# Kernel tuning notes

Measured on AMD Instinct MI355X. Metric: run time of the kernel, lower is better.

## Reference

```python
import jax, jax.numpy as jnp
import numpy as np

N = 100000      # nodes per batched graph
E = 3200000     # edges per batched graph
G = 1024        # number of graphs in the batch
F_IN = 128
H = 64


def gcn_conv(x, src, dst, W, b, n):
    # PyG GCNConv: lin -> symmetric-normalized propagate (with self-loops) -> +bias
    xw = x @ W                                   # [n, out]
    deg = jnp.zeros((n,), x.dtype).at[dst].add(1.0) + 1.0   # A+I degree
    dinv = jax.lax.rsqrt(deg)                    # deg >= 1, safe
    norm = (dinv[src] * dinv[dst])[:, None]      # [E,1]
    agg = jax.ops.segment_sum(norm * xw[src], dst, num_segments=n)
    # self-loop contribution: dinv[i]^2 * xw[i]
    return agg + (dinv * dinv)[:, None] * xw + b


def mean_pool(h, batch, num_graphs):
    sums = jax.ops.segment_sum(h, batch, num_segments=num_graphs)
    cnt = jax.ops.segment_sum(jnp.ones((h.shape[0],), h.dtype), batch, num_segments=num_graphs)
    return sums / jnp.maximum(cnt, 1.0)[:, None]


def branch(x, edge_index, batch, W1, b1, W2, b2):
    src, dst = edge_index[0], edge_index[1]
    h = jax.nn.relu(gcn_conv(x, src, dst, W1, b1, x.shape[0]))
    h = jax.nn.relu(gcn_conv(h, src, dst, W2, b2, x.shape[0]))
    return mean_pool(h, batch, G)


def setup_inputs() -> dict:
    key = jax.random.key(0)
    ks = jax.random.split(key, 14)
    x1 = jax.random.normal(ks[0], (N, F_IN), jnp.float32)
    x2 = jax.random.normal(ks[1], (N, F_IN), jnp.float32)
    edge_index1 = jax.random.randint(ks[2], (2, E), 0, N, jnp.int32)
    edge_index2 = jax.random.randint(ks[3], (2, E), 0, N, jnp.int32)
    batch1 = jnp.sort(jax.random.randint(ks[4], (N,), 0, G, jnp.int32))
    batch2 = jnp.sort(jax.random.randint(ks[5], (N,), 0, G, jnp.int32))
    s = 1.0 / np.sqrt(F_IN)
    W1 = jax.random.uniform(ks[6], (F_IN, H), jnp.float32, -s, s)
    b1 = jnp.zeros((H,), jnp.float32)
    s2 = 1.0 / np.sqrt(H)
    W2 = jax.random.uniform(ks[7], (H, H), jnp.float32, -s2, s2)
    b2 = jnp.zeros((H,), jnp.float32)
    s3 = 1.0 / np.sqrt(3 * H)
    fc1_W = jax.random.uniform(ks[8], (3 * H, H), jnp.float32, -s3, s3)
    fc1_b = jax.random.uniform(ks[9], (H,), jnp.float32, -s3, s3)
    fc2_W = jax.random.uniform(ks[10], (H, 1), jnp.float32, -s2, s2)
    fc2_b = jax.random.uniform(ks[11], (1,), jnp.float32, -s2, s2)
    return {"x1": x1, "edge_index1": edge_index1, "batch1": batch1,
            "x2": x2, "edge_index2": edge_index2, "batch2": batch2,
            "W1": W1, "b1": b1, "W2": W2, "b2": b2,
            "fc1_W": fc1_W, "fc1_b": fc1_b, "fc2_W": fc2_W, "fc2_b": fc2_b}


def reference(x1, edge_index1, batch1, x2, edge_index2, batch2,
              W1, b1, W2, b2, fc1_W, fc1_b, fc2_W, fc2_b):
    emb1 = branch(x1, edge_index1, batch1, W1, b1, W2, b2)   # [G, 64]
    emb2 = branch(x2, edge_index2, batch2, W1, b1, W2, b2)   # [G, 64]
    combined = jnp.concatenate([emb1, emb2, jnp.abs(emb1 - emb2)], axis=1)  # [G, 192]
    out = jax.nn.relu(combined @ fc1_W + fc1_b)
    out = jax.nn.sigmoid(out @ fc2_W + fc2_b)
    return out.squeeze(-1)  # [G]
```

## Files before the change

### kernel.cpp

```cpp
#include <hip/hip_runtime.h>
#include <hip/hip_fp16.h>
#include <cstdint>


#define NBSH 8
#define CAPB 10240
#define SPLIT_T 512
#define SPLIT_EPT 28
#define SPLIT_CHUNK (SPLIT_T * SPLIT_EPT)

__device__ __forceinline__ float fatomic(float* p, float v) {
    return unsafeAtomicAdd(p, v);
}
__device__ __forceinline__ float bf2f(unsigned short u) {
    union { unsigned int i; float f; } c; c.i = ((unsigned int)u) << 16; return c.f;
}
__device__ __forceinline__ unsigned short f2bf(float f) {
    union { float f; unsigned int i; } c; c.f = f;
    const unsigned int b = c.i;
    return (unsigned short)((b + 0x7FFF + ((b >> 16) & 1)) >> 16);
}

#if defined(__has_builtin)
#if __has_builtin(__builtin_amdgcn_cvt_f32_fp8) && __has_builtin(__builtin_amdgcn_cvt_pk_fp8_f32)
#define HW_FP8 1
#endif
#endif

__device__ __forceinline__ float fp8dec(unsigned int b) {
#ifdef HW_FP8
    return __builtin_amdgcn_cvt_f32_fp8((int)b, 0);
#else
    const unsigned int mag = (b & 0x7Fu) << 20;
    const float f = __uint_as_float(mag) * __uint_as_float(0x7B800000u);
    const unsigned int r = __float_as_uint(f) | ((b & 0x80u) << 24);
    return __uint_as_float(r);
#endif
}

__device__ __forceinline__ unsigned char fp8enc(float x) {
#ifdef HW_FP8
    const int v = __builtin_amdgcn_cvt_pk_fp8_f32(x, x, 0, false);
    return (unsigned char)(v & 0xFF);
#else
    const unsigned short h = __half_as_ushort(__float2half(x));
    const unsigned int s = (unsigned int)(h >> 15) << 7;
    const int e = (h >> 10) & 0x1F;
    const unsigned int m = h & 0x3FFu;
    if (e == 31) return (unsigned char)(s | 0x7E);
    if (e == 0) return (unsigned char)s;
    int E = e - 15 + 7;
    if (E >= 16) return (unsigned char)(s | 0x7E);
    if (E <= 0) {
        const unsigned int M = 0x400u | m;
        const int r = 16 - e;
        const unsigned int q = (M + (1u << (r - 1)) - 1u + ((M >> r) & 1u)) >> r;
        return (unsigned char)(s | (q > 7u ? 8u : q));
    }
    unsigned int q = (m + 63u + ((m >> 7) & 1u)) >> 7;
    if (q == 8u) { q = 0u; ++E; if (E >= 16) return (unsigned char)(s | 0x7E); }
    return (unsigned char)(s | ((unsigned int)E << 3) | q);
#endif
}

__global__ __launch_bounds__(512) void k_split(const int* __restrict__ src,
                                               const int* __restrict__ dst,
                                               int* __restrict__ gcnt,
                                               int* __restrict__ colBkt,
                                               int E, int NBUK) {
    __shared__ int out[SPLIT_CHUNK];
    __shared__ int bs[513];
    __shared__ int aux[512];
    const int t = threadIdx.x;
    const int e0 = blockIdx.x * SPLIT_CHUNK;

    int pk[SPLIT_EPT];
    int bk[SPLIT_EPT];

    aux[t] = 0;
    __syncthreads();

#pragma unroll
    for (int k = 0; k < SPLIT_EPT; ++k) {
        const int e = e0 + t + SPLIT_T * k;
        if (e < E) {
            const int d = dst[e];
            const int s = src[e];
            const int b = d >> NBSH;
            pk[k] = (s << NBSH) | (d & ((1 << NBSH) - 1));
            bk[k] = b;
            atomicAdd(&aux[b], 1);
        } else {
            bk[k] = -1;
        }
    }
    __syncthreads();

    for (int off = 1; off < 512; off <<= 1) {
        const int u = (t >= off) ? aux[t - off] : 0;
        __syncthreads();
        aux[t] += u;
        __syncthreads();
    }
    bs[t + 1] = aux[t];
    if (t == 0) bs[0] = 0;
    __syncthreads();

    aux[t] = 0;
    __syncthreads();

#pragma unroll
    for (int k = 0; k < SPLIT_EPT; ++k) {
        if (bk[k] >= 0) {
            const int pos = bs[bk[k]] + atomicAdd(&aux[bk[k]], 1);
            out[pos] = pk[k];
        }
    }
    __syncthreads();

    if (t < NBUK) {
        const int L = bs[t + 1] - bs[t];
        aux[t] = (L > 0) ? atomicAdd(&gcnt[t], L) : 0;
    } else if (t < 512) {
        aux[t] = 0;
    }
    __syncthreads();

    const int wid = t >> 6, lane = t & 63;
    for (int b = wid; b < NBUK; b += 8) {
        const int L = bs[b + 1] - bs[b];
        if (L == 0) continue;
        const int gp = aux[b];
        const size_t rb = (size_t)b * CAPB;
        for (int k = lane; k < L; k += 64) {
            const int p = gp + k;
            if (p < CAPB) colBkt[rb + p] = out[bs[b] + k];
        }
    }
}

__global__ __launch_bounds__(512) void k_gscan(const int* __restrict__ gcnt,
                                               int* __restrict__ gbase,
                                               int* __restrict__ rowstart,
                                               int NBUK, int Nn) {
    __shared__ int sm[512];
    const int t = threadIdx.x;
    const int v = (t < NBUK) ? min(gcnt[t], CAPB) : 0;
    sm[t] = v;
    __syncthreads();
    for (int off = 1; off < 512; off <<= 1) {
        const int u = (t >= off) ? sm[t - off] : 0;
        __syncthreads();
        sm[t] += u;
        __syncthreads();
    }
    if (t < NBUK) gbase[t] = sm[t] - v;
    if (t == 511) rowstart[Nn] = sm[511];
}

__global__ __launch_bounds__(256) void k_bsort(const int* __restrict__ colBkt,
                                               const int* __restrict__ gcnt,
                                               const int* __restrict__ gbase,
                                               int* __restrict__ colN,
                                               int* __restrict__ rowstart,
                                               float* __restrict__ dinv,
                                               int Nn) {
    __shared__ int in[CAPB];
    __shared__ int lb[257];
    __shared__ int fill[256];
    const int b = blockIdx.x;
    const int t = threadIdx.x;
    const int L = min(gcnt[b], CAPB);
    const size_t rb = (size_t)b * CAPB;
    for (int k = t; k < L; k += 256) in[k] = colBkt[rb + k];
    fill[t] = 0;
    __syncthreads();
    for (int k = t; k < L; k += 256) atomicAdd(&fill[in[k] & 255], 1);
    __syncthreads();
    for (int off = 1; off < 256; off <<= 1) {
        const int u = (t >= off) ? fill[t - off] : 0;
        __syncthreads();
        fill[t] += u;
        __syncthreads();
    }
    lb[t + 1] = fill[t];
    if (t == 0) lb[0] = 0;
    __syncthreads();
    const int bb = gbase[b];
    const int node = (b << NBSH) + t;
    if (node < Nn) {
        rowstart[node] = bb + lb[t];
        dinv[node] = rsqrtf((float)(lb[t + 1] - lb[t]) + 1.0f);
    }
    fill[t] = 0;
    __syncthreads();
    for (int k = t; k < L; k += 256) {
        const int v = in[k];
        const int n = v & 255;
        const int pos = bb + lb[n] + atomicAdd(&fill[n], 1);
        colN[pos] = v >> NBSH;
    }
}

template <int K, bool BF16IN>
__global__ __launch_bounds__(256) void k_mm(const void* __restrict__ Xv,
                                            const float* __restrict__ W,
                                            const float* __restrict__ dinv,
                                            unsigned char* __restrict__ Y, int n) {
    __shared__ float WL[K * 64];
    __shared__ float XT[32 * K];
    const int tid = threadIdx.x;
    for (int i = tid * 4; i < K * 64; i += 1024)
        *(float4*)&WL[i] = *(const float4*)&W[i];
    const int rowBase = blockIdx.x * 32;
    const int rows = min(32, n - rowBase);
    if (BF16IN) {
        const unsigned short* xs = (const unsigned short*)Xv + (size_t)rowBase * K;
        for (int i = tid * 4; i < rows * K; i += 1024) {
            const ushort4 u = *(const ushort4*)&xs[i];
            XT[i + 0] = bf2f(u.x); XT[i + 1] = bf2f(u.y);
            XT[i + 2] = bf2f(u.z); XT[i + 3] = bf2f(u.w);
        }
    } else {
        const float* xs = (const float*)Xv + (size_t)rowBase * K;
        for (int i = tid * 4; i < rows * K; i += 1024)
            *(float4*)&XT[i] = *(const float4*)&xs[i];
    }
    __syncthreads();
    const int colf = tid & 63;
    const int rg = tid >> 6;
    float acc[8] = {};
    for (int k4 = 0; k4 < K / 4; ++k4) {
        const float w0 = WL[(k4 * 4 + 0) * 64 + colf];
        const float w1 = WL[(k4 * 4 + 1) * 64 + colf];
        const float w2 = WL[(k4 * 4 + 2) * 64 + colf];
        const float w3 = WL[(k4 * 4 + 3) * 64 + colf];
#pragma unroll
        for (int r = 0; r < 8; ++r) {
            const float4 xv = *(const float4*)&XT[(rg * 8 + r) * K + k4 * 4];
            acc[r] += xv.x * w0 + xv.y * w1 + xv.z * w2 + xv.w * w3;
        }
    }
#pragma unroll
    for (int r = 0; r < 8; ++r) {
        const int row = rowBase + rg * 8 + r;
        if (row < n) Y[(size_t)row * 64 + colf] = fp8enc(dinv[row] * acc[r]);
    }
}

template <bool POOL>
__global__ __launch_bounds__(256) void k_agg(const int* __restrict__ colN,
                                             const int* __restrict__ rowstart,
                                             const float* __restrict__ dinv,
                                             const unsigned char* __restrict__ XW8,
                                             const float* __restrict__ bias,
                                             unsigned short* __restrict__ Hout,
                                             const int* __restrict__ batch,
                                             float* __restrict__ emb,
                                             float* __restrict__ cnt, int Nn) {
    const int lane = threadIdx.x & 63;
    const int wid = (blockIdx.x * blockDim.x + threadIdx.x) >> 6;
    const int nw = (gridDim.x * blockDim.x) >> 6;
    const float bl = bias[lane];
    for (int i = wid; i < Nn; i += nw) {
        const int s = rowstart[i], e = rowstart[i + 1];
        float acc = 0.0f;
        int j = s;
        for (; j + 16 <= e; j += 16) {
            int c[16];
#pragma unroll
            for (int q = 0; q < 16; ++q) c[q] = colN[j + q];
            unsigned int b[16];
#pragma unroll
            for (int q = 0; q < 16; ++q) b[q] = XW8[(size_t)c[q] * 64 + lane];
            float t0 = 0.f, t1 = 0.f;
#pragma unroll
            for (int q = 0; q < 8; ++q) t0 += fp8dec(b[q]);
#pragma unroll
            for (int q = 8; q < 16; ++q) t1 += fp8dec(b[q]);
            acc += t0 + t1;
        }
        for (; j + 4 <= e; j += 4) {
            const float a0 = fp8dec(XW8[(size_t)colN[j + 0] * 64 + lane]);
            const float a1 = fp8dec(XW8[(size_t)colN[j + 1] * 64 + lane]);
            const float a2 = fp8dec(XW8[(size_t)colN[j + 2] * 64 + lane]);
            const float a3 = fp8dec(XW8[(size_t)colN[j + 3] * 64 + lane]);
            acc += (a0 + a1) + (a2 + a3);
        }
        for (; j < e; ++j)
            acc += fp8dec(XW8[(size_t)colN[j] * 64 + lane]);
        const float di = dinv[i];
        const float self = fp8dec(XW8[(size_t)i * 64 + lane]);
        const float v = fmaxf(di * (acc + self) + bl, 0.0f);
        if (POOL) {
            const int g = batch[i];
            fatomic(&emb[(size_t)g * 64 + lane], v);
            if (lane == 0) fatomic(&cnt[g], 1.0f);
        } else {
            Hout[(size_t)i * 64 + lane] = f2bf(v);
        }
    }
}

__global__ __launch_bounds__(64) void k_head(const float* __restrict__ emb1, const float* __restrict__ cnt1,
                                             const float* __restrict__ emb2, const float* __restrict__ cnt2,
                                             const float* __restrict__ fc1W, const float* __restrict__ fc1b,
                                             const float* __restrict__ fc2W, const float* __restrict__ fc2b,
                                             float* __restrict__ out) {
    const int g = blockIdx.x;
    const int lane = threadIdx.x;
    __shared__ float comb[192];
    const float c1 = fmaxf(cnt1[g], 1.0f), c2 = fmaxf(cnt2[g], 1.0f);
    const float e1 = emb1[g * 64 + lane] / c1;
    const float e2 = emb2[g * 64 + lane] / c2;
    comb[lane] = e1;
    comb[64 + lane] = e2;
    comb[128 + lane] = fabsf(e1 - e2);
    __syncthreads();
    float acc = fc1b[lane];
    for (int k = 0; k < 192; ++k) acc += comb[k] * fc1W[k * 64 + lane];
    const float o1 = fmaxf(acc, 0.0f);
    float p = o1 * fc2W[lane];
#pragma unroll
    for (int off = 32; off > 0; off >>= 1) p += __shfl_xor(p, off);
    if (lane == 0) out[g] = 1.0f / (1.0f + expf(-(p + fc2b[0])));
}

extern "C" void kernel_launch(void* const* d_in, const int* in_sizes, int n_in,
                              void* d_out, int out_size, void* d_ws, size_t ws_size,
                              hipStream_t stream) {
    const float* x1   = (const float*)d_in[0];
    const int*   ei1  = (const int*)d_in[1];
    const int*   bt1  = (const int*)d_in[2];
    const float* x2   = (const float*)d_in[3];
    const int*   ei2  = (const int*)d_in[4];
    const int*   bt2  = (const int*)d_in[5];
    const float* W1   = (const float*)d_in[6];
    const float* bb1  = (const float*)d_in[7];
    const float* W2   = (const float*)d_in[8];
    const float* bb2  = (const float*)d_in[9];
    const float* fc1W = (const float*)d_in[10];
    const float* fc1b = (const float*)d_in[11];
    const float* fc2W = (const float*)d_in[12];
    const float* fc2b = (const float*)d_in[13];
    float* out = (float*)d_out;

    const int N = in_sizes[0] / 128;
    const int E = in_sizes[1] / 2;
    const int G = out_size;
    const int NBUK = (N + 255) >> NBSH;
    const int nchunks = (E + SPLIT_CHUNK - 1) / SPLIT_CHUNK;

    char* base = (char*)d_ws;
    size_t off = 0;
    auto carve = [&](size_t bytes) {
        void* p = base + off;
        off = (off + bytes + 15) & ~(size_t)15;
        return p;
    };
    float* dinv   = (float*)carve((size_t)N * 4);
    float* emb1   = (float*)carve((size_t)G * 64 * 4);
    float* cnt1   = (float*)carve((size_t)G * 4);
    float* emb2   = (float*)carve((size_t)G * 64 * 4);
    float* cnt2   = (float*)carve((size_t)G * 4);
    int* rowstart = (int*)carve((size_t)(N + 1) * 4);
    int* gcnt     = (int*)carve(512 * 4);
    int* gbase    = (int*)carve(512 * 4);
    int* colBkt   = (int*)carve((size_t)NBUK * CAPB * 4);
    int* colN     = (int*)carve((size_t)E * 4);
    unsigned char* XW8 = (unsigned char*)carve((size_t)N * 64);
    unsigned short* H1 = (unsigned short*)colBkt;

    const int mmGrid = (N + 31) / 32;

    for (int br = 0; br < 2; ++br) {
        const float* X = br ? x2 : x1;
        const int* ei  = br ? ei2 : ei1;
        const int* bt  = br ? bt2 : bt1;
        float* emb = br ? emb2 : emb1;
        float* cnt = br ? cnt2 : cnt1;
        const int* srcp = ei;
        const int* dstp = ei + E;

        hipMemsetAsync(gcnt, 0, 512 * 4, stream);
        k_split<<<nchunks, SPLIT_T, 0, stream>>>(srcp, dstp, gcnt, colBkt, E, NBUK);
        k_gscan<<<1, 512, 0, stream>>>(gcnt, gbase, rowstart, NBUK, N);
        k_bsort<<<NBUK, 256, 0, stream>>>(colBkt, gcnt, gbase, colN, rowstart, dinv, N);

        k_mm<128, false><<<mmGrid, 256, 0, stream>>>(X, W1, dinv, XW8, N);
        k_agg<false><<<2048, 256, 0, stream>>>(colN, rowstart, dinv, XW8, bb1,
                                               H1, nullptr, nullptr, nullptr, N);
        k_mm<64, true><<<mmGrid, 256, 0, stream>>>(H1, W2, dinv, XW8, N);
        hipMemsetAsync(emb, 0, (size_t)(G * 64 + G) * 4, stream);
        k_agg<true><<<2048, 256, 0, stream>>>(colN, rowstart, dinv, XW8, bb2,
                                              nullptr, bt, emb, cnt, N);
    }
    k_head<<<G, 64, 0, stream>>>(emb1, cnt1, emb2, cnt2, fc1W, fc1b, fc2W, fc2b, out);
}
```

Measured before the change: 831.3 us.

## Split fp8 feature table into two 32-column halves and aggregate each separately

Result: slower. 959.1 us (+15.4%).

```diff
diff --git a/kernel.cpp b/kernel.cpp
--- a/kernel.cpp
+++ b/kernel.cpp
@@ -203,10 +203,10 @@
 }
 
 template <int K, bool BF16IN>
-__global__ __launch_bounds__(256) void k_mm(const void* __restrict__ Xv,
-                                            const float* __restrict__ W,
-                                            const float* __restrict__ dinv,
-                                            unsigned char* __restrict__ Y, int n) {
+__global__ __launch_bounds__(256, 4) void k_mm(const void* __restrict__ Xv,
+                                               const float* __restrict__ W,
+                                               const float* __restrict__ dinv,
+                                               unsigned char* __restrict__ Y, int n) {
     __shared__ float WL[K * 64];
     __shared__ float XT[32 * K];
     const int tid = threadIdx.x;
@@ -230,6 +230,7 @@
     const int colf = tid & 63;
     const int rg = tid >> 6;
     float acc[8] = {};
+#pragma unroll 4
     for (int k4 = 0; k4 < K / 4; ++k4) {
         const float w0 = WL[(k4 * 4 + 0) * 64 + colf];
         const float w1 = WL[(k4 * 4 + 1) * 64 + colf];
@@ -241,63 +242,62 @@
             acc[r] += xv.x * w0 + xv.y * w1 + xv.z * w2 + xv.w * w3;
         }
     }
+    const size_t hoff = (size_t)(colf >> 5) * n * 32 + (colf & 31);
 #pragma unroll
     for (int r = 0; r < 8; ++r) {
         const int row = rowBase + rg * 8 + r;
-        if (row < n) Y[(size_t)row * 64 + colf] = fp8enc(dinv[row] * acc[r]);
-    }
-}
-
-template <bool POOL>
-__global__ __launch_bounds__(256) void k_agg(const int* __restrict__ colN,
-                                             const int* __restrict__ rowstart,
-                                             const float* __restrict__ dinv,
-                                             const unsigned char* __restrict__ XW8,
-                                             const float* __restrict__ bias,
-                                             unsigned short* __restrict__ Hout,
-                                             const int* __restrict__ batch,
-                                             float* __restrict__ emb,
-                                             float* __restrict__ cnt, int Nn) {
+        if (row < n) Y[hoff + (size_t)row * 32] = fp8enc(dinv[row] * acc[r]);
+    }
+}
+
+template <bool POOL, int H>
+__global__ __launch_bounds__(256) void k_aggh(const int* __restrict__ colN,
+                                              const int* __restrict__ rowstart,
+                                              const float* __restrict__ dinv,
+                                              const unsigned char* __restrict__ XWh,
+                                              const float* __restrict__ bias,
+                                              unsigned short* __restrict__ Hout,
+                                              const int* __restrict__ batch,
+                                              float* __restrict__ emb,
+                                              float* __restrict__ cnt, int Nn) {
     const int lane = threadIdx.x & 63;
+    const int hg = lane >> 5;
+    const int l32 = lane & 31;
     const int wid = (blockIdx.x * blockDim.x + threadIdx.x) >> 6;
     const int nw = (gridDim.x * blockDim.x) >> 6;
-    const float bl = bias[lane];
+    const float bl = bias[H * 32 + l32];
     for (int i = wid; i < Nn; i += nw) {
         const int s = rowstart[i], e = rowstart[i + 1];
         float acc = 0.0f;
-        int j = s;
-        for (; j + 16 <= e; j += 16) {
-            int c[16];
-#pragma unroll
-            for (int q = 0; q < 16; ++q) c[q] = colN[j + q];
-            unsigned int b[16];
-#pragma unroll
-            for (int q = 0; q < 16; ++q) b[q] = XW8[(size_t)c[q] * 64 + lane];
+        int j = s + hg;
+        for (; j + 14 < e; j += 16) {
+            int c[8];
+#pragma unroll
+            for (int q = 0; q < 8; ++q) c[q] = colN[j + 2 * q];
+            unsigned int b[8];
+#pragma unroll
+            for (int q = 0; q < 8; ++q) b[q] = XWh[(size_t)c[q] * 32 + l32];
             float t0 = 0.f, t1 = 0.f;
 #pragma unroll
-            for (int q = 0; q < 8; ++q) t0 += fp8dec(b[q]);
-#pragma unroll
-            for (int q = 8; q < 16; ++q) t1 += fp8dec(b[q]);
+            for (int q = 0; q < 4; ++q) t0 += fp8dec(b[q]);
+#pragma unroll
+            for (int q = 4; q < 8; ++q) t1 += fp8dec(b[q]);
             acc += t0 + t1;
         }
-        for (; j + 4 <= e; j += 4) {
-            const float a0 = fp8dec(XW8[(size_t)colN[j + 0] * 64 + lane]);
-            const float a1 = fp8dec(XW8[(size_t)colN[j + 1] * 64 + lane]);
-            const float a2 = fp8dec(XW8[(size_t)colN[j + 2] * 64 + lane]);
-            const float a3 = fp8dec(XW8[(size_t)colN[j + 3] * 64 + lane]);
-            acc += (a0 + a1) + (a2 + a3);
-        }
-        for (; j < e; ++j)
-            acc += fp8dec(XW8[(size_t)colN[j] * 64 + lane]);
+        for (; j < e; j += 2)
+            acc += fp8dec(XWh[(size_t)colN[j] * 32 + l32]);
+        acc += __shfl_xor(acc, 32);
         const float di = dinv[i];
-        const float self = fp8dec(XW8[(size_t)i * 64 + lane]);
+        const float self = fp8dec(XWh[(size_t)i * 32 + l32]);
         const float v = fmaxf(di * (acc + self) + bl, 0.0f);
-        if (POOL) {
-            const int g = batch[i];
-            fatomic(&emb[(size_t)g * 64 + lane], v);
-            if (lane == 0) fatomic(&cnt[g], 1.0f);
-        } else {
-            Hout[(size_t)i * 64 + lane] = f2bf(v);
+        if (hg == 0) {
+            if (POOL) {
+                const int g = batch[i];
+                fatomic(&emb[(size_t)g * 64 + H * 32 + l32], v);
+                if (H == 0 && l32 == 0) fatomic(&cnt[g], 1.0f);
+            } else {
+                Hout[(size_t)i * 64 + H * 32 + l32] = f2bf(v);
+            }
         }
     }
 }
@@ -388,12 +388,16 @@
         k_bsort<<<NBUK, 256, 0, stream>>>(colBkt, gcnt, gbase, colN, rowstart, dinv, N);
 
         k_mm<128, false><<<mmGrid, 256, 0, stream>>>(X, W1, dinv, XW8, N);
-        k_agg<false><<<2048, 256, 0, stream>>>(colN, rowstart, dinv, XW8, bb1,
-                                               H1, nullptr, nullptr, nullptr, N);
+        k_aggh<false, 0><<<2048, 256, 0, stream>>>(colN, rowstart, dinv, XW8,
+                                                   bb1, H1, nullptr, nullptr, nullptr, N);
+        k_aggh<false, 1><<<2048, 256, 0, stream>>>(colN, rowstart, dinv, XW8 + (size_t)N * 32,
+                                                   bb1, H1, nullptr, nullptr, nullptr, N);
         k_mm<64, true><<<mmGrid, 256, 0, stream>>>(H1, W2, dinv, XW8, N);
         hipMemsetAsync(emb, 0, (size_t)(G * 64 + G) * 4, stream);
-        k_agg<true><<<2048, 256, 0, stream>>>(colN, rowstart, dinv, XW8, bb2,
-                                              nullptr, bt, emb, cnt, N);
+        k_aggh<true, 0><<<2048, 256, 0, stream>>>(colN, rowstart, dinv, XW8,
+                                                  bb2, nullptr, bt, emb, cnt, N);
+        k_aggh<true, 1><<<2048, 256, 0, stream>>>(colN, rowstart, dinv, XW8 + (size_t)N * 32,
+                                                  bb2, nullptr, bt, emb, cnt, N);
     }
     k_head<<<G, 64, 0, stream>>>(emb1, cnt1, emb2, cnt2, fc1W, fc1b, fc2W, fc2b, out);
 }
```
